# Optimization experiments

Measured on AMD Instinct MI355X. Metric: run time of the kernel, lower is better.

The kernel has to match this reference:

```python
import jax, jax.numpy as jnp
import numpy as np

N_NODES = 40000


def _gcn_conv(x, edge_index, W, b):
    """PyG GCNConv: add self-loops, symmetric degree normalization,
    linear transform, gather-scale-scatter aggregation, bias."""
    n = x.shape[0]
    loops = jnp.arange(n, dtype=edge_index.dtype)
    src = jnp.concatenate([edge_index[0], loops])  # [E+N]
    dst = jnp.concatenate([edge_index[1], loops])  # [E+N]
    ones = jnp.ones(src.shape[0], dtype=x.dtype)
    deg = jax.ops.segment_sum(ones, dst, num_segments=n)  # in-degree incl. self-loop
    dinv = jnp.where(deg > 0, jax.lax.rsqrt(deg), 0.0)
    norm = dinv[src] * dinv[dst]  # [E+N]
    h = x @ W  # [n, out]
    msg = h[src] * norm[:, None]  # [E+N, out] gather + scale
    out = jax.ops.segment_sum(msg, dst, num_segments=n)  # scatter-add
    return out + b


def setup_inputs() -> dict:
    key = jax.random.key(0)
    k = jax.random.split(key, 6)
    n, din, dh, dout = N_NODES, 128, 128, 64
    x = jax.random.normal(k[0], (n, din), dtype=jnp.float32)
    edge_index = jax.random.randint(k[1], (2, 640000), 0, n, dtype=jnp.int64)
    W1 = jax.random.normal(k[2], (din, dh), dtype=jnp.float32) / np.sqrt(din)
    b1 = jnp.zeros((dh,), dtype=jnp.float32)
    W2 = jax.random.normal(k[3], (dh, dout), dtype=jnp.float32) / np.sqrt(dh)
    b2 = jnp.zeros((dout,), dtype=jnp.float32)
    return {"x": x, "edge_index": edge_index, "W1": W1, "b1": b1, "W2": W2, "b2": b2}


def reference(x, edge_index, W1, b1, W2, b2):
    h = jax.nn.relu(_gcn_conv(x, edge_index, W1, b1))
    return _gcn_conv(h, edge_index, W2, b2)
```

## Files before the change

### kernel.cpp

```cpp
#include <hip/hip_runtime.h>
#include <hip/hip_fp16.h>


#define N_NODES 40000
#define DIN 128
#define DH 128
#define DOUT 64
#define NEDGES 640000
#define CAP 64
#define NBUCKET 2560
#define I4_PER_CHUNK 500
#define NODES_PER_XCD 5000
#define NCVT 1250
#define NWT 8

typedef _Float16 f16x8 __attribute__((ext_vector_type(8)));
typedef float f32x4 __attribute__((ext_vector_type(4)));

__global__ __launch_bounds__(256) void k_bkt_cvt(
    const float* __restrict__ x, _Float16* __restrict__ xh,
    const int4* __restrict__ src4, const int4* __restrict__ dst4,
    int* __restrict__ deg, unsigned short* __restrict__ ssrc,
    const float* __restrict__ W1, const float* __restrict__ W2,
    _Float16* __restrict__ WT1, _Float16* __restrict__ WT2)
{
    if (blockIdx.x < NBUCKET) {
        const int xg = blockIdx.x & 7;
        const int c  = blockIdx.x >> 3;
        const int lo = xg * NODES_PER_XCD, hi = lo + NODES_PER_XCD;
        const int e0 = c * I4_PER_CHUNK, e1 = e0 + I4_PER_CHUNK;
        for (int e = e0 + threadIdx.x; e < e1; e += 256) {
            int4 d = dst4[e];
            int4 s = src4[e];
            if (d.x >= lo && d.x < hi) {
                int p = atomicAdd(&deg[d.x], 1);
                if (p < CAP) ssrc[d.x * CAP + p] = (unsigned short)s.x;
            }
            if (d.y >= lo && d.y < hi) {
                int p = atomicAdd(&deg[d.y], 1);
                if (p < CAP) ssrc[d.y * CAP + p] = (unsigned short)s.y;
            }
            if (d.z >= lo && d.z < hi) {
                int p = atomicAdd(&deg[d.z], 1);
                if (p < CAP) ssrc[d.z * CAP + p] = (unsigned short)s.z;
            }
            if (d.w >= lo && d.w < hi) {
                int p = atomicAdd(&deg[d.w], 1);
                if (p < CAP) ssrc[d.w * CAP + p] = (unsigned short)s.w;
            }
        }
    } else if (blockIdx.x < NBUCKET + NCVT) {
        const size_t base = ((size_t)(blockIdx.x - NBUCKET) * 256 + threadIdx.x) * 16;
        float4 a0 = *(const float4*)(x + base);
        float4 a1 = *(const float4*)(x + base + 4);
        float4 a2 = *(const float4*)(x + base + 8);
        float4 a3 = *(const float4*)(x + base + 12);
        f16x8 o0 = { (_Float16)a0.x, (_Float16)a0.y, (_Float16)a0.z, (_Float16)a0.w,
                     (_Float16)a1.x, (_Float16)a1.y, (_Float16)a1.z, (_Float16)a1.w };
        f16x8 o1 = { (_Float16)a2.x, (_Float16)a2.y, (_Float16)a2.z, (_Float16)a2.w,
                     (_Float16)a3.x, (_Float16)a3.y, (_Float16)a3.z, (_Float16)a3.w };
        *(f16x8*)(xh + base)     = o0;
        *(f16x8*)(xh + base + 8) = o1;
    } else {
        const int b = blockIdx.x - NBUCKET - NCVT;
        for (int i = b * 256 + threadIdx.x; i < DIN * DH; i += NWT * 256) {
            int k = i >> 7, nn = i & 127;
            WT1[nn * DIN + k] = (_Float16)W1[i];
        }
        for (int i = b * 256 + threadIdx.x; i < DH * DOUT; i += NWT * 256) {
            int k = i >> 6, nn = i & 63;
            WT2[nn * DH + k] = (_Float16)W2[i];
        }
    }
}

__global__ __launch_bounds__(1024) void k_agg_g12(
    const int* __restrict__ deg, const unsigned short* __restrict__ ssrc,
    const __half* __restrict__ xh, const float* __restrict__ b1,
    const _Float16* __restrict__ WT1, const _Float16* __restrict__ WT2,
    __half* __restrict__ h2)
{
    __shared__ _Float16 ys[16][136];
    __shared__ _Float16 zs[16][136];
    const int w = threadIdx.x >> 6;
    const int lane = threadIdx.x & 63;
    const int node0 = blockIdx.x * 16;
    const int node = node0 + w;
    const __half2* hp = (const __half2*)xh;

    const int dg = deg[node];
    const int cnt = min(dg, CAP);
    const float dn = rsqrtf((float)(dg + 1));
    float2 self = __half22float2(hp[(size_t)node * 64 + lane]);
    float2 acc = { self.x * dn, self.y * dn };
    const uint4* bin4 = (const uint4*)(ssrc + (size_t)node * CAP);
    int e = 0;
    for (; e + 8 <= cnt; e += 8) {
        uint4 pk = bin4[e >> 3];
        int s0 = pk.x & 0xFFFF, s1 = pk.x >> 16;
        int s2 = pk.y & 0xFFFF, s3 = pk.y >> 16;
        int s4 = pk.z & 0xFFFF, s5 = pk.z >> 16;
        int s6 = pk.w & 0xFFFF, s7 = pk.w >> 16;
        float w0 = rsqrtf((float)(deg[s0] + 1)), w1 = rsqrtf((float)(deg[s1] + 1));
        float w2 = rsqrtf((float)(deg[s2] + 1)), w3 = rsqrtf((float)(deg[s3] + 1));
        float w4 = rsqrtf((float)(deg[s4] + 1)), w5 = rsqrtf((float)(deg[s5] + 1));
        float w6 = rsqrtf((float)(deg[s6] + 1)), w7 = rsqrtf((float)(deg[s7] + 1));
        float2 v0 = __half22float2(hp[(size_t)s0 * 64 + lane]);
        float2 v1 = __half22float2(hp[(size_t)s1 * 64 + lane]);
        float2 v2 = __half22float2(hp[(size_t)s2 * 64 + lane]);
        float2 v3 = __half22float2(hp[(size_t)s3 * 64 + lane]);
        float2 v4 = __half22float2(hp[(size_t)s4 * 64 + lane]);
        float2 v5 = __half22float2(hp[(size_t)s5 * 64 + lane]);
        float2 v6 = __half22float2(hp[(size_t)s6 * 64 + lane]);
        float2 v7 = __half22float2(hp[(size_t)s7 * 64 + lane]);
        acc.x += (v0.x * w0 + v1.x * w1) + (v2.x * w2 + v3.x * w3)
               + (v4.x * w4 + v5.x * w5) + (v6.x * w6 + v7.x * w7);
        acc.y += (v0.y * w0 + v1.y * w1) + (v2.y * w2 + v3.y * w3)
               + (v4.y * w4 + v5.y * w5) + (v6.y * w6 + v7.y * w7);
    }
    for (; e < cnt; ++e) {
        int s = ssrc[(size_t)node * CAP + e];
        float wv = rsqrtf((float)(deg[s] + 1));
        float2 v = __half22float2(hp[(size_t)s * 64 + lane]);
        acc.x += v.x * wv; acc.y += v.y * wv;
    }
    ys[w][2 * lane]     = (_Float16)(dn * acc.x);
    ys[w][2 * lane + 1] = (_Float16)(dn * acc.y);
    __syncthreads();

    const int m = lane & 15, quad = lane >> 4;
    if (w < 8) {
        f32x4 acc1 = (f32x4){0.f, 0.f, 0.f, 0.f};
#pragma unroll
        for (int ks = 0; ks < 4; ++ks) {
            f16x8 a = *(const f16x8*)&ys[m][ks * 32 + quad * 8];
            f16x8 b = *(const f16x8*)(WT1 + (size_t)(w * 16 + m) * DIN + ks * 32 + quad * 8);
            acc1 = __builtin_amdgcn_mfma_f32_16x16x32_f16(a, b, acc1, 0, 0, 0);
        }
        float bias = b1[w * 16 + m];
#pragma unroll
        for (int r = 0; r < 4; ++r) {
            float v = acc1[r] + bias;
            zs[quad * 4 + r][w * 16 + m] = (_Float16)(v > 0.f ? v : 0.f);
        }
    }
    __syncthreads();

    if (w < 4) {
        f32x4 acc2 = (f32x4){0.f, 0.f, 0.f, 0.f};
#pragma unroll
        for (int ks = 0; ks < 4; ++ks) {
            f16x8 a = *(const f16x8*)&zs[m][ks * 32 + quad * 8];
            f16x8 b = *(const f16x8*)(WT2 + (size_t)(w * 16 + m) * DH + ks * 32 + quad * 8);
            acc2 = __builtin_amdgcn_mfma_f32_16x16x32_f16(a, b, acc2, 0, 0, 0);
        }
#pragma unroll
        for (int r = 0; r < 4; ++r) {
            int nrow = node0 + quad * 4 + r;
            float dnr = rsqrtf((float)(deg[nrow] + 1));
            h2[(size_t)nrow * DOUT + w * 16 + m] = (__half)(acc2[r] * dnr);
        }
    }
}

__global__ __launch_bounds__(256) void k_agg2(
    const int* __restrict__ deg, const unsigned short* __restrict__ ssrc,
    const __half* __restrict__ h, const float* __restrict__ b2,
    float* __restrict__ out)
{
    const int node = blockIdx.x * 4 + (threadIdx.x >> 6);
    const int lane = threadIdx.x & 63;
    const int half = lane >> 5;
    const int lp = lane & 31;
    const int dg = deg[node];
    const int cnt = min(dg, CAP);
    const __half2* hp = (const __half2*)h;

    float2 acc;
    if (half == 0) acc = __half22float2(hp[(size_t)node * 32 + lp]);
    else           acc = make_float2(0.f, 0.f);

    const uint4* bin4 = (const uint4*)(ssrc + (size_t)node * CAP);
    int e = 0;
    for (; e + 8 <= cnt; e += 8) {
        uint4 pk = bin4[e >> 3];
        int sa, sb, sc, sd;
        if (half == 0) { sa = pk.x & 0xFFFF; sb = pk.y & 0xFFFF;
                         sc = pk.z & 0xFFFF; sd = pk.w & 0xFFFF; }
        else           { sa = pk.x >> 16;    sb = pk.y >> 16;
                         sc = pk.z >> 16;    sd = pk.w >> 16; }
        float2 v0 = __half22float2(hp[(size_t)sa * 32 + lp]);
        float2 v1 = __half22float2(hp[(size_t)sb * 32 + lp]);
        float2 v2 = __half22float2(hp[(size_t)sc * 32 + lp]);
        float2 v3 = __half22float2(hp[(size_t)sd * 32 + lp]);
        acc.x += (v0.x + v1.x) + (v2.x + v3.x);
        acc.y += (v0.y + v1.y) + (v2.y + v3.y);
    }
    for (; e + 2 <= cnt; e += 2) {
        int s = ssrc[(size_t)node * CAP + e + half];
        float2 v = __half22float2(hp[(size_t)s * 32 + lp]);
        acc.x += v.x; acc.y += v.y;
    }
    if (e < cnt) {
        int s = ssrc[(size_t)node * CAP + e];
        if (half == 0) {
            float2 v = __half22float2(hp[(size_t)s * 32 + lp]);
            acc.x += v.x; acc.y += v.y;
        }
    }
    acc.x += __shfl_xor(acc.x, 32);
    acc.y += __shfl_xor(acc.y, 32);
    if (half == 0) {
        float dn = rsqrtf((float)(dg + 1));
        float2 o;
        o.x = dn * acc.x + b2[2 * lp];
        o.y = dn * acc.y + b2[2 * lp + 1];
        *(float2*)&out[(size_t)node * 64 + 2 * lp] = o;
    }
}

extern "C" void kernel_launch(void* const* d_in, const int* in_sizes, int n_in,
                              void* d_out, int out_size, void* d_ws, size_t ws_size,
                              hipStream_t stream) {
    const float* x  = (const float*)d_in[0];
    const int*   ei = (const int*)d_in[1];
    const float* W1 = (const float*)d_in[2];
    const float* b1 = (const float*)d_in[3];
    const float* W2 = (const float*)d_in[4];
    const float* b2 = (const float*)d_in[5];
    float* out = (float*)d_out;

    const int n = N_NODES, E = NEDGES;
    const int* src = ei;
    const int* dst = ei + E;

    char* ws = (char*)d_ws;
    int*            deg  = (int*)(ws + 0);
    _Float16*       WT1  = (_Float16*)(ws + 163840);
    _Float16*       WT2  = (_Float16*)(ws + 196608);
    unsigned short* ssrc = (unsigned short*)(ws + 212992);
    _Float16*       xh   = (_Float16*)(ws + 5332992);
    __half*         h2   = (__half*)(ws + 15572992);

    hipMemsetAsync(deg, 0, N_NODES * sizeof(int), stream);
    k_bkt_cvt <<<NBUCKET + NCVT + NWT, 256, 0, stream>>>(x, xh, (const int4*)src,
                                                         (const int4*)dst, deg, ssrc,
                                                         W1, W2, WT1, WT2);
    k_agg_g12 <<<n / 16, 1024, 0, stream>>>(deg, ssrc, (const __half*)xh, b1,
                                            WT1, WT2, h2);
    k_agg2    <<<n / 4,  256, 0, stream>>>(deg, ssrc, h2, b2, out);
}
```

Measured before the change: 181.0 us.

## Map multiple nodes per wavefront with 16-byte gathers in both aggregation kernels

Both aggregation kernels now assign several nodes to each wavefront: 4 nodes of 16 lanes in layer 1 and 8 nodes of 8 lanes in layer 2. Each lane gathers 8 fp16 features with one 16-byte load, where before a whole wave handled one node with 4-byte loads. The layer-1 block shrinks from 1024 to 256 threads, and each wave now issues two MFMA tiles for the first GEMM and one for the second. The aim is fewer, wider memory transactions and less per-wave loop overhead. The cost is divergence, since each group loops to the maximum degree in its wave and masks the padded edges.

```diff
diff --git a/kernel.cpp b/kernel.cpp
--- a/kernel.cpp
+++ b/kernel.cpp
@@ -74,79 +74,86 @@
     }
 }
 
-__global__ __launch_bounds__(1024) void k_agg_g12(
+__global__ __launch_bounds__(256) void k_agg_g12(
     const int* __restrict__ deg, const unsigned short* __restrict__ ssrc,
-    const __half* __restrict__ xh, const float* __restrict__ b1,
+    const _Float16* __restrict__ xh, const float* __restrict__ b1,
     const _Float16* __restrict__ WT1, const _Float16* __restrict__ WT2,
-    __half* __restrict__ h2)
+    _Float16* __restrict__ h2)
 {
     __shared__ _Float16 ys[16][136];
     __shared__ _Float16 zs[16][136];
     const int w = threadIdx.x >> 6;
     const int lane = threadIdx.x & 63;
+    const int g  = lane >> 4;
+    const int gl = lane & 15;
     const int node0 = blockIdx.x * 16;
-    const int node = node0 + w;
-    const __half2* hp = (const __half2*)xh;
+    const int node = node0 + w * 4 + g;
 
     const int dg = deg[node];
     const int cnt = min(dg, CAP);
     const float dn = rsqrtf((float)(dg + 1));
-    float2 self = __half22float2(hp[(size_t)node * 64 + lane]);
-    float2 acc = { self.x * dn, self.y * dn };
-    const uint4* bin4 = (const uint4*)(ssrc + (size_t)node * CAP);
-    int e = 0;
-    for (; e + 8 <= cnt; e += 8) {
-        uint4 pk = bin4[e >> 3];
-        int s0 = pk.x & 0xFFFF, s1 = pk.x >> 16;
-        int s2 = pk.y & 0xFFFF, s3 = pk.y >> 16;
-        int s4 = pk.z & 0xFFFF, s5 = pk.z >> 16;
-        int s6 = pk.w & 0xFFFF, s7 = pk.w >> 16;
-        float w0 = rsqrtf((float)(deg[s0] + 1)), w1 = rsqrtf((float)(deg[s1] + 1));
-        float w2 = rsqrtf((float)(deg[s2] + 1)), w3 = rsqrtf((float)(deg[s3] + 1));
-        float w4 = rsqrtf((float)(deg[s4] + 1)), w5 = rsqrtf((float)(deg[s5] + 1));
-        float w6 = rsqrtf((float)(deg[s6] + 1)), w7 = rsqrtf((float)(deg[s7] + 1));
-        float2 v0 = __half22float2(hp[(size_t)s0 * 64 + lane]);
-        float2 v1 = __half22float2(hp[(size_t)s1 * 64 + lane]);
-        float2 v2 = __half22float2(hp[(size_t)s2 * 64 + lane]);
-        float2 v3 = __half22float2(hp[(size_t)s3 * 64 + lane]);
-        float2 v4 = __half22float2(hp[(size_t)s4 * 64 + lane]);
-        float2 v5 = __half22float2(hp[(size_t)s5 * 64 + lane]);
-        float2 v6 = __half22float2(hp[(size_t)s6 * 64 + lane]);
-        float2 v7 = __half22float2(hp[(size_t)s7 * 64 + lane]);
-        acc.x += (v0.x * w0 + v1.x * w1) + (v2.x * w2 + v3.x * w3)
-               + (v4.x * w4 + v5.x * w5) + (v6.x * w6 + v7.x * w7);
-        acc.y += (v0.y * w0 + v1.y * w1) + (v2.y * w2 + v3.y * w3)
-               + (v4.y * w4 + v5.y * w5) + (v6.y * w6 + v7.y * w7);
-    }
-    for (; e < cnt; ++e) {
-        int s = ssrc[(size_t)node * CAP + e];
-        float wv = rsqrtf((float)(deg[s] + 1));
-        float2 v = __half22float2(hp[(size_t)s * 64 + lane]);
-        acc.x += v.x * wv; acc.y += v.y * wv;
-    }
-    ys[w][2 * lane]     = (_Float16)(dn * acc.x);
-    ys[w][2 * lane + 1] = (_Float16)(dn * acc.y);
+
+    float ac[8];
+    {
+        f16x8 self = *(const f16x8*)(xh + (size_t)node * DIN + gl * 8);
+#pragma unroll
+        for (int j = 0; j < 8; ++j) ac[j] = dn * (float)self[j];
+    }
+    int mc = cnt;
+    mc = max(mc, __shfl_xor(mc, 16));
+    mc = max(mc, __shfl_xor(mc, 32));
+
+    const unsigned short* bin = ssrc + (size_t)node * CAP;
+    for (int e = 0; e < mc; e += 4) {
+        unsigned long long pk = *(const unsigned long long*)(bin + e);
+        int s0 = (int)(pk & 0xFFFF),         s1 = (int)((pk >> 16) & 0xFFFF);
+        int s2 = (int)((pk >> 32) & 0xFFFF), s3 = (int)((pk >> 48) & 0xFFFF);
+        s0 = (e + 0 < cnt) ? s0 : 0;
+        s1 = (e + 1 < cnt) ? s1 : 0;
+        s2 = (e + 2 < cnt) ? s2 : 0;
+        s3 = (e + 3 < cnt) ? s3 : 0;
+        f16x8 r0 = *(const f16x8*)(xh + (size_t)s0 * DIN + gl * 8);
+        f16x8 r1 = *(const f16x8*)(xh + (size_t)s1 * DIN + gl * 8);
+        f16x8 r2 = *(const f16x8*)(xh + (size_t)s2 * DIN + gl * 8);
+        f16x8 r3 = *(const f16x8*)(xh + (size_t)s3 * DIN + gl * 8);
+        float w0 = (e + 0 < cnt) ? rsqrtf((float)(deg[s0] + 1)) : 0.f;
+        float w1 = (e + 1 < cnt) ? rsqrtf((float)(deg[s1] + 1)) : 0.f;
+        float w2 = (e + 2 < cnt) ? rsqrtf((float)(deg[s2] + 1)) : 0.f;
+        float w3 = (e + 3 < cnt) ? rsqrtf((float)(deg[s3] + 1)) : 0.f;
+#pragma unroll
+        for (int j = 0; j < 8; ++j)
+            ac[j] += (w0 * (float)r0[j] + w1 * (float)r1[j])
+                   + (w2 * (float)r2[j] + w3 * (float)r3[j]);
+    }
+    {
+        f16x8 o;
+#pragma unroll
+        for (int j = 0; j < 8; ++j) o[j] = (_Float16)(dn * ac[j]);
+        *(f16x8*)&ys[w * 4 + g][gl * 8] = o;
+    }
     __syncthreads();
 
     const int m = lane & 15, quad = lane >> 4;
-    if (w < 8) {
+#pragma unroll
+    for (int t = 0; t < 2; ++t) {
+        const int nt = w * 2 + t;
         f32x4 acc1 = (f32x4){0.f, 0.f, 0.f, 0.f};
 #pragma unroll
         for (int ks = 0; ks < 4; ++ks) {
             f16x8 a = *(const f16x8*)&ys[m][ks * 32 + quad * 8];
-            f16x8 b = *(const f16x8*)(WT1 + (size_t)(w * 16 + m) * DIN + ks * 32 + quad * 8);
+            f16x8 b = *(const f16x8*)(WT1 + (size_t)(nt * 16 + m) * DIN + ks * 32 + quad * 8);
             acc1 = __builtin_amdgcn_mfma_f32_16x16x32_f16(a, b, acc1, 0, 0, 0);
         }
-        float bias = b1[w * 16 + m];
+        float bias = b1[nt * 16 + m];
 #pragma unroll
         for (int r = 0; r < 4; ++r) {
             float v = acc1[r] + bias;
-            zs[quad * 4 + r][w * 16 + m] = (_Float16)(v > 0.f ? v : 0.f);
+            zs[quad * 4 + r][nt * 16 + m] = (_Float16)(v > 0.f ? v : 0.f);
         }
     }
     __syncthreads();
 
-    if (w < 4) {
+    {
         f32x4 acc2 = (f32x4){0.f, 0.f, 0.f, 0.f};
 #pragma unroll
         for (int ks = 0; ks < 4; ++ks) {
@@ -158,65 +165,68 @@
         for (int r = 0; r < 4; ++r) {
             int nrow = node0 + quad * 4 + r;
             float dnr = rsqrtf((float)(deg[nrow] + 1));
-            h2[(size_t)nrow * DOUT + w * 16 + m] = (__half)(acc2[r] * dnr);
+            h2[(size_t)nrow * DOUT + w * 16 + m] = (_Float16)(acc2[r] * dnr);
         }
     }
 }
 
 __global__ __launch_bounds__(256) void k_agg2(
     const int* __restrict__ deg, const unsigned short* __restrict__ ssrc,
-    const __half* __restrict__ h, const float* __restrict__ b2,
+    const _Float16* __restrict__ h2, const float* __restrict__ b2,
     float* __restrict__ out)
 {
-    const int node = blockIdx.x * 4 + (threadIdx.x >> 6);
+    const int w = threadIdx.x >> 6;
     const int lane = threadIdx.x & 63;
-    const int half = lane >> 5;
-    const int lp = lane & 31;
+    const int g  = lane >> 3;
+    const int gl = lane & 7;
+    const int node = blockIdx.x * 32 + w * 8 + g;
+
     const int dg = deg[node];
     const int cnt = min(dg, CAP);
-    const __half2* hp = (const __half2*)h;
-
-    float2 acc;
-    if (half == 0) acc = __half22float2(hp[(size_t)node * 32 + lp]);
-    else           acc = make_float2(0.f, 0.f);
-
-    const uint4* bin4 = (const uint4*)(ssrc + (size_t)node * CAP);
-    int e = 0;
-    for (; e + 8 <= cnt; e += 8) {
-        uint4 pk = bin4[e >> 3];
-        int sa, sb, sc, sd;
-        if (half == 0) { sa = pk.x & 0xFFFF; sb = pk.y & 0xFFFF;
-                         sc = pk.z & 0xFFFF; sd = pk.w & 0xFFFF; }
-        else           { sa = pk.x >> 16;    sb = pk.y >> 16;
-                         sc = pk.z >> 16;    sd = pk.w >> 16; }
-        float2 v0 = __half22float2(hp[(size_t)sa * 32 + lp]);
-        float2 v1 = __half22float2(hp[(size_t)sb * 32 + lp]);
-        float2 v2 = __half22float2(hp[(size_t)sc * 32 + lp]);
-        float2 v3 = __half22float2(hp[(size_t)sd * 32 + lp]);
-        acc.x += (v0.x + v1.x) + (v2.x + v3.x);
-        acc.y += (v0.y + v1.y) + (v2.y + v3.y);
-    }
-    for (; e + 2 <= cnt; e += 2) {
-        int s = ssrc[(size_t)node * CAP + e + half];
-        float2 v = __half22float2(hp[(size_t)s * 32 + lp]);
-        acc.x += v.x; acc.y += v.y;
-    }
-    if (e < cnt) {
-        int s = ssrc[(size_t)node * CAP + e];
-        if (half == 0) {
-            float2 v = __half22float2(hp[(size_t)s * 32 + lp]);
-            acc.x += v.x; acc.y += v.y;
-        }
-    }
-    acc.x += __shfl_xor(acc.x, 32);
-    acc.y += __shfl_xor(acc.y, 32);
-    if (half == 0) {
-        float dn = rsqrtf((float)(dg + 1));
-        float2 o;
-        o.x = dn * acc.x + b2[2 * lp];
-        o.y = dn * acc.y + b2[2 * lp + 1];
-        *(float2*)&out[(size_t)node * 64 + 2 * lp] = o;
-    }
+    const float dn = rsqrtf((float)(dg + 1));
+
+    float ac[8];
+    {
+        f16x8 self = *(const f16x8*)(h2 + (size_t)node * DOUT + gl * 8);
+#pragma unroll
+        for (int j = 0; j < 8; ++j) ac[j] = (float)self[j];
+    }
+    int mc = cnt;
+    mc = max(mc, __shfl_xor(mc, 8));
+    mc = max(mc, __shfl_xor(mc, 16));
+    mc = max(mc, __shfl_xor(mc, 32));
+
+    const unsigned short* bin = ssrc + (size_t)node * CAP;
+    for (int e = 0; e < mc; e += 4) {
+        unsigned long long pk = *(const unsigned long long*)(bin + e);
+        int s0 = (int)(pk & 0xFFFF),         s1 = (int)((pk >> 16) & 0xFFFF);
+        int s2 = (int)((pk >> 32) & 0xFFFF), s3 = (int)((pk >> 48) & 0xFFFF);
+        s0 = (e + 0 < cnt) ? s0 : 0;
+        s1 = (e + 1 < cnt) ? s1 : 0;
+        s2 = (e + 2 < cnt) ? s2 : 0;
+        s3 = (e + 3 < cnt) ? s3 : 0;
+        float m0 = (e + 0 < cnt) ? 1.f : 0.f;
+        float m1 = (e + 1 < cnt) ? 1.f : 0.f;
+        float m2 = (e + 2 < cnt) ? 1.f : 0.f;
+        float m3 = (e + 3 < cnt) ? 1.f : 0.f;
+        f16x8 r0 = *(const f16x8*)(h2 + (size_t)s0 * DOUT + gl * 8);
+        f16x8 r1 = *(const f16x8*)(h2 + (size_t)s1 * DOUT + gl * 8);
+        f16x8 r2 = *(const f16x8*)(h2 + (size_t)s2 * DOUT + gl * 8);
+        f16x8 r3 = *(const f16x8*)(h2 + (size_t)s3 * DOUT + gl * 8);
+#pragma unroll
+        for (int j = 0; j < 8; ++j)
+            ac[j] += (m0 * (float)r0[j] + m1 * (float)r1[j])
+                   + (m2 * (float)r2[j] + m3 * (float)r3[j]);
+    }
+    float4 ba = *(const float4*)(b2 + gl * 8);
+    float4 bb = *(const float4*)(b2 + gl * 8 + 4);
+    float4 o0 = { dn * ac[0] + ba.x, dn * ac[1] + ba.y,
+                  dn * ac[2] + ba.z, dn * ac[3] + ba.w };
+    float4 o1 = { dn * ac[4] + bb.x, dn * ac[5] + bb.y,
+                  dn * ac[6] + bb.z, dn * ac[7] + bb.w };
+    float* orow = out + (size_t)node * DOUT + gl * 8;
+    *(float4*)orow = o0;
+    *(float4*)(orow + 4) = o1;
 }
 
 extern "C" void kernel_launch(void* const* d_in, const int* in_sizes, int n_in,
@@ -240,13 +250,12 @@
     _Float16*       WT2  = (_Float16*)(ws + 196608);
     unsigned short* ssrc = (unsigned short*)(ws + 212992);
     _Float16*       xh   = (_Float16*)(ws + 5332992);
-    __half*         h2   = (__half*)(ws + 15572992);
+    _Float16*       h2   = (_Float16*)(ws + 15572992);
 
     hipMemsetAsync(deg, 0, N_NODES * sizeof(int), stream);
     k_bkt_cvt <<<NBUCKET + NCVT + NWT, 256, 0, stream>>>(x, xh, (const int4*)src,
                                                          (const int4*)dst, deg, ssrc,
                                                          W1, W2, WT1, WT2);
-    k_agg_g12 <<<n / 16, 1024, 0, stream>>>(deg, ssrc, (const __half*)xh, b1,
-                                            WT1, WT2, h2);
-    k_agg2    <<<n / 4,  256, 0, stream>>>(deg, ssrc, h2, b2, out);
-}
+    k_agg_g12 <<<n / 16, 256, 0, stream>>>(deg, ssrc, xh, b1, WT1, WT2, h2);
+    k_agg2    <<<n / 32, 256, 0, stream>>>(deg, ssrc, h2, b2, out);
+}
```

Measured after the change: 166.7 us. 7.9% less time.
